# Performance work log

Hardware: AMD Instinct MI355X
Metric: run time of the kernel (lower is better)

Reference implementation:

```python
import jax, jax.numpy as jnp
import numpy as np

L, H, D, N, M, P, C, IMG, B = 12, 12, 768, 197, 3072, 16, 3, 224, 16
SKIP_AT = (3, 6, 9, 12)


def pos_emb(n, d):
    i = jnp.arange(n, dtype=jnp.float32)[:, None]
    j = jnp.arange(d)[None, :]
    je = (j // 2) * 2  # j for even, j-1 for odd
    ang = i / jnp.power(10000.0, je.astype(jnp.float32) / d)
    return jnp.where(j % 2 == 0, jnp.sin(ang), jnp.cos(ang))  # [n, d]


def layer_norm(x, g, b):
    mu = x.mean(-1, keepdims=True)
    var = x.var(-1, keepdims=True)
    return (x - mu) / jnp.sqrt(var + 1e-5) * g + b


def setup_inputs() -> dict:
    key = jax.random.key(0)
    ks = jax.random.split(key, 16)
    s = 0.02
    f32 = jnp.float32
    return {
        "images": jax.random.normal(ks[0], (B, C, IMG, IMG), f32),
        "class_token": jax.random.uniform(ks[1], (1, D), f32),
        "Wp": jax.random.normal(ks[2], (D, P * P * C), f32) * s,
        "bp": jnp.zeros((D,), f32),
        "Wq": jax.random.normal(ks[3], (L, H, D, D), f32) * s,
        "bq": jnp.zeros((L, H, D), f32),
        "Wk": jax.random.normal(ks[4], (L, H, D, D), f32) * s,
        "bk": jnp.zeros((L, H, D), f32),
        "Wv": jax.random.normal(ks[5], (L, H, D, D), f32) * s,
        "bv": jnp.zeros((L, H, D), f32),
        "Wm": jax.random.normal(ks[6], (L, N, H * N), f32) * s,
        "bm": jnp.zeros((L, N), f32),
        "g1": jnp.ones((L, D), f32),
        "be1": jnp.zeros((L, D), f32),
        "W1": jax.random.normal(ks[7], (L, M, D), f32) * s,
        "b1": jnp.zeros((L, M), f32),
        "W2": jax.random.normal(ks[8], (L, D, M), f32) * s,
        "b2": jnp.zeros((L, D), f32),
        "g2": jnp.ones((L, D), f32),
        "be2": jnp.zeros((L, D), f32),
    }


def reference(images, class_token, Wp, bp, Wq, bq, Wk, bk, Wv, bv, Wm, bm,
              g1, be1, W1, b1, W2, b2, g2, be2):
    b = images.shape[0]
    Hn, Wn = IMG // P, IMG // P
    # einops 'b c (patch_x h) (patch_y w) -> b (h w) (patch_x patch_y c)'
    x = images.reshape(b, C, P, Hn, P, Wn).transpose(0, 3, 5, 2, 4, 1)
    patches = x.reshape(b, Hn * Wn, P * P * C)
    tokens = patches @ Wp.T + bp  # [b, N-1, D]
    cls = jnp.broadcast_to(class_token[None], (b, 1, D))
    out = jnp.concatenate([cls, tokens], axis=1) + pos_emb(N, D)[None]
    scale = 1.0 / jnp.sqrt(jnp.float32(N - 1))
    skips = []
    for l in range(L):
        x0 = out
        q = jnp.einsum('bnd,hed->bhne', x0, Wq[l]) + bq[l][None, :, None, :]
        k = jnp.einsum('bnd,hed->bhne', x0, Wk[l]) + bk[l][None, :, None, :]
        v = jnp.einsum('bnd,hed->bhne', x0, Wv[l]) + bv[l][None, :, None, :]
        attn = jax.nn.softmax(jnp.einsum('bhne,bhme->bhnm', q, k) * scale, axis=-1)
        o = jnp.einsum('bhnm,bhme->bhne', attn, v).reshape(b, H * N, D)
        # transpose -> [b, D, H*N], Linear(H*N -> N), transpose back
        msa = jnp.einsum('bfd,nf->bnd', o, Wm[l]) + bm[l][None, :, None]
        x1 = layer_norm(x0 + msa, g1[l], be1[l])
        hdn = jax.nn.gelu(x1 @ W1[l].T + b1[l], approximate=False)
        out = layer_norm(x1 + (hdn @ W2[l].T + b2[l]), g2[l], be2[l])
        if l + 1 in SKIP_AT:
            skips.append(out[:, 1:, :])
    return (out[:, 1:, :], *skips)
```

## Files before the change

kernel.cpp:

```cpp
#include <hip/hip_runtime.h>
#include <cstdint>
#include <cstddef>

typedef __bf16 bf16;
typedef __bf16 bf16x8 __attribute__((ext_vector_type(8)));
typedef float f32x4 __attribute__((ext_vector_type(4)));

#define DEVINL __device__ __forceinline__

typedef const __attribute__((address_space(1))) void* as1cv;
typedef __attribute__((address_space(3))) void* as3v;

DEVINL void gload16(const bf16* g, bf16* l) {
    __builtin_amdgcn_global_load_lds((as1cv)g, (as3v)l, 16, 0, 0);
}

static constexpr int Lh = 12, Hh = 12, Dh = 768, Nh = 197, Mh = 3072, Bh = 16;
static constexpr int BN   = Bh * Nh;
static constexpr int NPAT = Bh * 196;
static constexpr int HD   = Hh * Dh;
static constexpr int QKN  = 2 * HD;
static constexpr int NP   = 256;
static constexpr int FHN  = Hh * Nh;
static constexpr int FP   = 2368;
static constexpr size_t SEC = (size_t)Bh * 196 * Dh;
static constexpr long LSqk = (long)QKN * Dh;
static constexpr long PART = (long)BN * Dh;

template<int AF32, int BF32, int OUTBF, int BIAS, int ACT, int ZFILL>
__global__ __launch_bounds__(256, 3) void gemm_bt(
    const void* __restrict__ Av, long sAy, long sAz, int lda,
    const void* __restrict__ Bv, long sBy, long sBz, int ldb,
    void* __restrict__ Cv, long sCy, long sCz, int ldc,
    const float* __restrict__ bias, long sBiasY,
    int Mv, int Nv, int K, int tilesN, int kChunk)
{
    __shared__ __align__(16) bf16 Asm[128 * 32];
    __shared__ __align__(16) bf16 Bsm[128 * 32];
    const int bx = blockIdx.x;
    const int tm = bx / tilesN, tn = bx % tilesN;
    const long aoff = (long)blockIdx.y * sAy + (long)blockIdx.z * sAz + (long)tm * 128 * lda;
    const long boff = (long)blockIdx.y * sBy + (long)blockIdx.z * sBz + (long)tn * 128 * ldb;
    const int tid = threadIdx.x;
    const int lane = tid & 63, wid = tid >> 6;
    const int ar = tid >> 2, ac = (tid & 3) << 3;
    const bf16* Ag = (const bf16*)Av + aoff + (long)ar * lda + ac;
    const bf16* Bg = (const bf16*)Bv + boff + (long)ar * ldb + ac;
    const float* Af = (const float*)Av + aoff + (long)ar * lda + ac;
    const float* Bf = (const float*)Bv + boff + (long)ar * ldb + ac;
    bf16* lA = Asm + wid * 512;
    bf16* lB = Bsm + wid * 512;
    const int mw = (wid >> 1) * 64, nw = (wid & 1) * 64;
    const int fr = lane & 15, fq = lane >> 4;
    const int kBeg = kChunk ? blockIdx.y * kChunk : 0;
    const int kEnd = kChunk ? min(K, kBeg + kChunk) : K;
    f32x4 acc[4][4] = {};
    for (int k0 = kBeg; k0 < kEnd; k0 += 32) {
        if (AF32) {
            const float* p0 = Af + k0;
            const float* p1 = p0 + (long)64 * lda;
            f32x4 a0 = *(const f32x4*)p0, a1 = *(const f32x4*)(p0 + 4);
            f32x4 a2 = *(const f32x4*)p1, a3 = *(const f32x4*)(p1 + 4);
            bf16x8 r0, r1;
#pragma unroll
            for (int i = 0; i < 4; i++) { r0[i] = (bf16)a0[i]; r0[i + 4] = (bf16)a1[i];
                                          r1[i] = (bf16)a2[i]; r1[i + 4] = (bf16)a3[i]; }
            *(bf16x8*)&Asm[ar * 32 + ac] = r0;
            *(bf16x8*)&Asm[(ar + 64) * 32 + ac] = r1;
        } else {
            gload16(Ag + k0, lA);
            gload16(Ag + (long)64 * lda + k0, lA + 2048);
        }
        if (BF32) {
            const float* p0 = Bf + k0;
            const float* p1 = p0 + (long)64 * ldb;
            f32x4 a0 = *(const f32x4*)p0, a1 = *(const f32x4*)(p0 + 4);
            f32x4 a2 = *(const f32x4*)p1, a3 = *(const f32x4*)(p1 + 4);
            bf16x8 r0, r1;
#pragma unroll
            for (int i = 0; i < 4; i++) { r0[i] = (bf16)a0[i]; r0[i + 4] = (bf16)a1[i];
                                          r1[i] = (bf16)a2[i]; r1[i + 4] = (bf16)a3[i]; }
            *(bf16x8*)&Bsm[ar * 32 + ac] = r0;
            *(bf16x8*)&Bsm[(ar + 64) * 32 + ac] = r1;
        } else {
            gload16(Bg + k0, lB);
            gload16(Bg + (long)64 * ldb + k0, lB + 2048);
        }
        __syncthreads();
        bf16x8 af[4], bv[4];
#pragma unroll
        for (int i = 0; i < 4; i++) af[i] = *(const bf16x8*)&Asm[(mw + i * 16 + fr) * 32 + (fq << 3)];
#pragma unroll
        for (int j = 0; j < 4; j++) bv[j] = *(const bf16x8*)&Bsm[(nw + j * 16 + fr) * 32 + (fq << 3)];
#pragma unroll
        for (int i = 0; i < 4; i++)
#pragma unroll
            for (int j = 0; j < 4; j++)
                acc[i][j] = __builtin_amdgcn_mfma_f32_16x16x32_bf16(af[i], bv[j], acc[i][j], 0, 0, 0);
        __syncthreads();
    }
    const long cb = (long)blockIdx.y * sCy + (long)blockIdx.z * sCz;
    const float* biasp = bias ? bias + (long)blockIdx.y * sBiasY : nullptr;
#pragma unroll
    for (int i = 0; i < 4; i++) {
        const int row0 = tm * 128 + mw + i * 16 + fq * 4;
#pragma unroll
        for (int j = 0; j < 4; j++) {
            const int col = tn * 128 + nw + j * 16 + fr;
            const bool cok = (col < Nv);
            if (!cok && !ZFILL) continue;
            float bc = (BIAS == 1 && cok) ? biasp[col] : 0.f;
#pragma unroll
            for (int r = 0; r < 4; r++) {
                const int rr = row0 + r;
                if (rr >= Mv) continue;
                float v;
                if (cok) {
                    v = acc[i][j][r];
                    if (BIAS == 1) v += bc;
                    if (BIAS == 2) v += biasp[rr];
                    if (ACT) v = 0.5f * v * (1.f + erff(v * 0.70710678118654752f));
                } else v = 0.f;
                const long ci = cb + (long)rr * ldc + col;
                if (OUTBF) ((bf16*)Cv)[ci] = (bf16)v;
                else       ((float*)Cv)[ci] = v;
            }
        }
    }
}

__global__ __launch_bounds__(256) void cvt_k(const float* __restrict__ in, bf16* __restrict__ out, long n) {
    const long i = ((long)blockIdx.x * 256 + threadIdx.x) * 8;
    if (i >= n) return;
    f32x4 a = *(const f32x4*)(in + i);
    f32x4 b = *(const f32x4*)(in + i + 4);
    bf16x8 r;
#pragma unroll
    for (int j = 0; j < 4; j++) { r[j] = (bf16)a[j]; r[j + 4] = (bf16)b[j]; }
    *(bf16x8*)(out + i) = r;
}

__global__ __launch_bounds__(256) void cvt_s_k(const float* __restrict__ in, bf16* __restrict__ out,
                                               long perLayer, long dstStride, long dstOff, long total) {
    const long i = ((long)blockIdx.x * 256 + threadIdx.x) * 8;
    if (i >= total) return;
    const long l = i / perLayer, r = i % perLayer;
    f32x4 a = *(const f32x4*)(in + i);
    f32x4 b = *(const f32x4*)(in + i + 4);
    bf16x8 v;
#pragma unroll
    for (int j = 0; j < 4; j++) { v[j] = (bf16)a[j]; v[j + 4] = (bf16)b[j]; }
    *(bf16x8*)(out + l * dstStride + dstOff + r) = v;
}

__global__ void qkbias_k(const float* __restrict__ bq, const float* __restrict__ bk, float* __restrict__ dst) {
    const int idx = blockIdx.x * 256 + threadIdx.x;
    if (idx >= Lh * QKN) return;
    const int l = idx / QKN, c = idx % QKN;
    dst[idx] = (c < HD) ? bq[l * HD + c] : bk[l * HD + c - HD];
}

__global__ void patch_k(const float* __restrict__ images, bf16* __restrict__ patches) {
    const long idx = (long)blockIdx.x * 256 + threadIdx.x;
    if (idx >= (long)NPAT * Dh) return;
    const int r = (int)(idx / Dh), f = (int)(idx % Dh);
    const int b = r / 196, pi = r % 196, h = pi / 14, w = pi % 14;
    const int px = f / 48, rem = f % 48, py = rem / 3, c = rem % 3;
    patches[idx] = (bf16)images[(((long)(b * 3 + c) * 224) + px * 14 + h) * 224 + py * 14 + w];
}

__global__ void assemble_k(const float* __restrict__ tokens, const float* __restrict__ cls,
                           float* __restrict__ x, bf16* __restrict__ xbf) {
    const long idx = (long)blockIdx.x * 256 + threadIdx.x;
    if (idx >= (long)BN * Dh) return;
    const int r = (int)(idx / Dh), d = (int)(idx % Dh);
    const int b = r / Nh, n = r % Nh;
    const int je = d & ~1;
    const float ang = (float)n / powf(10000.f, (float)je / 768.f);
    const float pe = (d & 1) ? cosf(ang) : sinf(ang);
    const float val = (n == 0) ? (cls[d] + pe)
                               : (tokens[((long)b * 196 + (n - 1)) * Dh + d] + pe);
    x[idx] = val;
    xbf[idx] = (bf16)val;
}

__global__ void wmpad_k(const float* __restrict__ Wm, bf16* __restrict__ WmP) {
    const long idx = (long)blockIdx.x * 256 + threadIdx.x;
    if (idx >= (long)Lh * 256 * FP) return;
    const int l = (int)(idx / (256 * FP));
    const int rem = (int)(idx % (256 * FP));
    const int n = rem / FP, f = rem % FP;
    bf16 v = (bf16)0.f;
    if (n < Nh && f < FHN) v = (bf16)Wm[((long)l * Nh + n) * FHN + f];
    WmP[idx] = v;
}

__global__ void otpad_k(bf16* __restrict__ oT, int cb) {
    const int idx = blockIdx.x * 256 + threadIdx.x;
    if (idx >= cb * Dh * 4) return;
    const int b = idx / (Dh * 4), rem = idx % (Dh * 4), e = rem / 4, f = rem % 4;
    oT[((long)b * Dh + e) * FP + FHN + f] = (bf16)0.f;
}

__global__ __launch_bounds__(256) void softmax_k(const float* __restrict__ S, bf16* __restrict__ P) {
    const int tid = threadIdx.x, lane = tid & 63, wv = tid >> 6;
    const long rr = (long)blockIdx.x * 4 + wv;
    const int bh = (int)(rr / Nh), n = (int)(rr % Nh);
    const float* s = S + ((long)bh * Nh + n) * NP;
    bf16* p = P + ((long)bh * NP + n) * NP;
    float v[4]; float mx = -1e30f;
#pragma unroll
    for (int i = 0; i < 4; i++) {
        const int c = lane + i * 64;
        const float t = (c < Nh) ? s[c] * (1.f / 14.f) : -1e30f;
        v[i] = t; mx = fmaxf(mx, t);
    }
    for (int o = 32; o; o >>= 1) mx = fmaxf(mx, __shfl_xor(mx, o));
    float sum = 0.f;
#pragma unroll
    for (int i = 0; i < 4; i++) {
        const int c = lane + i * 64;
        v[i] = (c < Nh) ? expf(v[i] - mx) : 0.f;
        sum += v[i];
    }
    for (int o = 32; o; o >>= 1) sum += __shfl_xor(sum, o);
    const float inv = 1.f / sum;
#pragma unroll
    for (int i = 0; i < 4; i++) p[lane + i * 64] = (bf16)(v[i] * inv);
}

template<int BIAS_ROW, int NPART>
__global__ __launch_bounds__(256) void add_ln_k(
    const float* __restrict__ in1, const float* __restrict__ in2, long pstride,
    const float* __restrict__ bias, const float* __restrict__ gamma, const float* __restrict__ beta,
    float* __restrict__ outF, bf16* __restrict__ outBF,
    float* __restrict__ dst0, float* __restrict__ dst1)
{
    const int r = blockIdx.x;
    const int b = r / Nh, n = r % Nh;
    const long base = (long)r * Dh;
    const int tid = threadIdx.x;
    const float rowb = BIAS_ROW ? bias[n] : 0.f;
    float v[3]; float s = 0.f, s2 = 0.f;
#pragma unroll
    for (int i = 0; i < 3; i++) {
        const int d = tid + 256 * i;
        float t = in1[base + d] + (BIAS_ROW ? rowb : bias[d]);
#pragma unroll
        for (int pp = 0; pp < NPART; pp++) t += in2[pp * pstride + base + d];
        v[i] = t; s += t; s2 += t * t;
    }
    for (int o = 32; o; o >>= 1) { s += __shfl_xor(s, o); s2 += __shfl_xor(s2, o); }
    __shared__ float red[8];
    const int lane = tid & 63, wv = tid >> 6;
    if (lane == 0) { red[wv] = s; red[4 + wv] = s2; }
    __syncthreads();
    s  = red[0] + red[1] + red[2] + red[3];
    s2 = red[4] + red[5] + red[6] + red[7];
    const float mu = s * (1.f / 768.f);
    const float var = s2 * (1.f / 768.f) - mu * mu;
    const float rs = rsqrtf(var + 1e-5f);
    const long ob = ((long)b * 196 + (n - 1)) * Dh;
#pragma unroll
    for (int i = 0; i < 3; i++) {
        const int d = tid + 256 * i;
        const float y = (v[i] - mu) * rs * gamma[d] + beta[d];
        outF[base + d] = y;
        outBF[base + d] = (bf16)y;
        if (n > 0) {
            if (dst0) dst0[ob + d] = y;
            if (dst1) dst1[ob + d] = y;
        }
    }
}

static inline size_t al256(size_t x) { return (x + 255) & ~(size_t)255; }

extern "C" void kernel_launch(void* const* d_in, const int* in_sizes, int n_in,
                              void* d_out, int out_size, void* d_ws, size_t ws_size,
                              hipStream_t stream) {
    (void)in_sizes; (void)n_in; (void)out_size;
    const float* images = (const float*)d_in[0];
    const float* cls    = (const float*)d_in[1];
    const float* Wp     = (const float*)d_in[2];
    const float* bp     = (const float*)d_in[3];
    const float* Wq     = (const float*)d_in[4];
    const float* bq     = (const float*)d_in[5];
    const float* Wk     = (const float*)d_in[6];
    const float* bk     = (const float*)d_in[7];
    const float* Wv     = (const float*)d_in[8];
    const float* bv     = (const float*)d_in[9];
    const float* Wm     = (const float*)d_in[10];
    const float* bm     = (const float*)d_in[11];
    const float* g1     = (const float*)d_in[12];
    const float* be1    = (const float*)d_in[13];
    const float* W1     = (const float*)d_in[14];
    const float* b1     = (const float*)d_in[15];
    const float* W2     = (const float*)d_in[16];
    const float* b2     = (const float*)d_in[17];
    const float* g2     = (const float*)d_in[18];
    const float* be2    = (const float*)d_in[19];
    float* out = (float*)d_out;

    const size_t xB    = al256(3152ull * 768 * 4);
    const size_t xbfB  = al256(3328ull * 768 * 2);
    const size_t x1B   = al256(3152ull * 768 * 4);
    const size_t x1bfB = al256(3200ull * 768 * 2);
    const size_t msaB  = al256(4ull * PART * 4);
    const size_t mlp2B = al256(4ull * PART * 4);
    const size_t wmpB  = al256(12ull * 256 * FP * 2);
    const size_t qkbB  = al256((size_t)Lh * QKN * 4);
    const size_t persistB = xB + xbfB + x1B + x1bfB + msaB + mlp2B + wmpB + qkbB;
    const size_t hdnB  = al256(3200ull * 3072 * 2);
    const size_t preB  = al256(3200ull * 768 * 2) + al256(3136ull * 768 * 4);
    const size_t wqkvB = al256((size_t)Lh * HD * Dh * 2);
    const size_t w12B  = al256((size_t)Lh * Mh * Dh * 2);
    const size_t wpB   = al256(768ull * 768 * 2);
    const size_t weightsB = 3 * wqkvB + 2 * w12B + wpB;

    auto chunk_bytes = [&](int cb, size_t& qbB_o, size_t& vtB_o, size_t& sB_o) -> size_t {
        const size_t qbRows = (size_t)((cb * 197 + 127) / 128 + 1) * 128;
        size_t qbB = al256(qbRows * HD * 2);
        size_t vtB = al256((size_t)cb * Hh * Dh * NP * 2);
        size_t sB  = al256((size_t)cb * Hh * Nh * NP * 4);
        size_t c = 2 * qbB + vtB + sB;
        if (c < hdnB) c = hdnB;
        if (c < preB) c = preB;
        qbB_o = qbB; vtB_o = vtB; sB_o = sB;
        return c;
    };
    const size_t margin = (size_t)(8u << 20);
    const size_t pBf  = al256((size_t)Bh * Hh * NP * NP * 2);
    const size_t otBf = al256((size_t)Bh * Dh * FP * 2);
    size_t qbBf, vtBf, sBf;
    size_t chunkF = chunk_bytes(16, qbBf, vtBf, sBf) + pBf + otBf;
    bool fused = (chunkF + persistB + weightsB + margin <= ws_size);

    int CB = 16; bool useCvt = true;
    size_t qbB, vtB, sB, chunkB;
    if (fused) {
        chunkB = chunkF; qbB = qbBf; vtB = vtBf; sB = sBf;
    } else {
        for (;;) {
            chunkB = chunk_bytes(CB, qbB, vtB, sB);
            if (chunkB + persistB + weightsB + margin <= ws_size) break;
            if (CB == 1) { useCvt = false; break; }
            CB >>= 1;
        }
        if (!useCvt) {
            CB = 16;
            for (;;) {
                chunkB = chunk_bytes(CB, qbB, vtB, sB);
                if (chunkB + persistB + margin <= ws_size || CB == 1) break;
                CB >>= 1;
            }
        }
    }

    char* wsb = (char*)d_ws;
    bf16*  qb  = (bf16*)wsb;
    bf16*  kb  = (bf16*)(wsb + qbB);
    bf16*  vT  = (bf16*)(wsb + 2 * qbB);
    float* S   = (float*)(wsb + 2 * qbB + vtB);
    bf16*  P2  = (bf16*)(wsb + 2 * qbB + vtB + sB);
    bf16*  oT2 = (bf16*)(wsb + 2 * qbB + vtB + sB + pBf);
    bf16*  oT  = fused ? oT2 : qb;
    bf16*  P   = fused ? P2  : kb;
    bf16*  hdn = (bf16*)wsb;
    bf16*  patches = (bf16*)wsb;
    float* tokens  = (float*)(wsb + al256(3200ull * 768 * 2));
    char* p = wsb + chunkB;
    float* x    = (float*)p; p += xB;
    bf16*  xbf  = (bf16*) p; p += xbfB;
    float* x1   = (float*)p; p += x1B;
    bf16*  x1bf = (bf16*) p; p += x1bfB;
    float* msaP = (float*)p; p += msaB;
    float* mlp2P= (float*)p; p += mlp2B;
    bf16*  WmP  = (bf16*) p; p += wmpB;
    float* qkbiasF = (float*)p; p += qkbB;
    bf16 *WqkB = nullptr, *WvB = nullptr, *W1B = nullptr, *W2B = nullptr, *WpB = nullptr;
    const bool cvt = fused || useCvt;
    if (cvt) {
        WqkB = (bf16*)p; p += 2 * wqkvB;
        WvB  = (bf16*)p; p += wqkvB;
        W1B  = (bf16*)p; p += w12B;
        W2B  = (bf16*)p; p += w12B;
        WpB  = (bf16*)p; p += wpB;
    }

    if (cvt) {
        const long nqkv = (long)Lh * HD * Dh;
        const long n12  = (long)Lh * Mh * Dh;
        const int gq = (int)((nqkv / 8 + 255) / 256);
        const int g12 = (int)((n12 / 8 + 255) / 256);
        cvt_s_k<<<gq, 256, 0, stream>>>(Wq, WqkB, (long)HD * Dh, LSqk, 0, nqkv);
        cvt_s_k<<<gq, 256, 0, stream>>>(Wk, WqkB, (long)HD * Dh, LSqk, (long)HD * Dh, nqkv);
        cvt_k<<<gq, 256, 0, stream>>>(Wv, WvB, nqkv);
        cvt_k<<<g12, 256, 0, stream>>>(W1, W1B, n12);
        cvt_k<<<g12, 256, 0, stream>>>(W2, W2B, n12);
        cvt_k<<<(768 * 768 / 8 + 255) / 256, 256, 0, stream>>>(Wp, WpB, 768 * 768);
        qkbias_k<<<(Lh * QKN + 255) / 256, 256, 0, stream>>>(bq, bk, qkbiasF);
    }

    patch_k<<<9408, 256, 0, stream>>>(images, patches);
    if (cvt)
        gemm_bt<0, 0, 0, 1, 0, 0><<<dim3(25 * 6), 256, 0, stream>>>(
            patches, 0, 0, 768, WpB, 0, 0, 768, tokens, 0, 0, 768, bp, 0, NPAT, 768, 768, 6, 0);
    else
        gemm_bt<0, 1, 0, 1, 0, 0><<<dim3(25 * 6), 256, 0, stream>>>(
            patches, 0, 0, 768, Wp, 0, 0, 768, tokens, 0, 0, 768, bp, 0, NPAT, 768, 768, 6, 0);
    assemble_k<<<9456, 256, 0, stream>>>(tokens, cls, x, xbf);
    wmpad_k<<<28416, 256, 0, stream>>>(Wm, WmP);
    if (fused) otpad_k<<<16 * 12, 256, 0, stream>>>(oT2, 16);

    const int NCH = 16 / CB;
    const int tilesQ = (CB * 197 + 127) / 128;

    for (int l = 0; l < 12; l++) {
        const float* Wq_l = Wq + (size_t)l * HD * Dh;
        const float* Wk_l = Wk + (size_t)l * HD * Dh;
        const float* Wv_l = Wv + (size_t)l * HD * Dh;
        const bf16* WqkB_l = cvt ? WqkB + (size_t)l * LSqk : nullptr;
        const bf16* WqB_l = WqkB_l;
        const bf16* WkB_l = cvt ? WqkB_l + (size_t)HD * Dh : nullptr;
        const bf16* WvB_l = cvt ? WvB + (size_t)l * HD * Dh : nullptr;
        const float* bq_l = bq + (size_t)l * HD;
        const float* bk_l = bk + (size_t)l * HD;
        const float* bv_l = bv + (size_t)l * HD;
        const bf16*  WmP_l = WmP + (size_t)l * 256 * FP;
        const float* bm_l = bm + (size_t)l * Nh;
        const float* g1_l = g1 + (size_t)l * Dh;  const float* be1_l = be1 + (size_t)l * Dh;
        const float* W1_l = W1 + (size_t)l * Mh * Dh; const float* b1_l = b1 + (size_t)l * Mh;
        const float* W2_l = W2 + (size_t)l * Dh * Mh; const float* b2_l = b2 + (size_t)l * Dh;
        const bf16* W1B_l = cvt ? W1B + (size_t)l * Mh * Dh : nullptr;
        const bf16* W2B_l = cvt ? W2B + (size_t)l * Mh * Dh : nullptr;
        const float* g2_l = g2 + (size_t)l * Dh;  const float* be2_l = be2 + (size_t)l * Dh;

        if (fused) {
            gemm_bt<0, 0, 1, 1, 0, 0><<<dim3(25 * 144), 256, 0, stream>>>(
                xbf, 0, 0, 768, WqkB_l, 0, 0, 768, qb, 0, 0, QKN,
                qkbiasF + (size_t)l * QKN, 0, BN, QKN, 768, 144, 0);
            gemm_bt<0, 0, 1, 2, 0, 1><<<dim3(12, 12, 16), 256, 0, stream>>>(
                WvB_l, (long)Dh * Dh, 0, 768,
                xbf, 0, (long)Nh * Dh, 768,
                vT, (long)Dh * NP, (long)Hh * Dh * NP, NP,
                bv_l, Dh, 768, Nh, 768, 2, 0);
            gemm_bt<0, 0, 0, 0, 0, 0><<<dim3(4, 12, 16), 256, 0, stream>>>(
                qb, 768, (long)Nh * QKN, QKN,
                qb + HD, 768, (long)Nh * QKN, QKN,
                S, (long)Nh * NP, (long)Hh * Nh * NP, NP,
                nullptr, 0, Nh, Nh, 768, 2, 0);
            softmax_k<<<16 * 591, 256, 0, stream>>>(S, P);
            gemm_bt<0, 0, 1, 0, 0, 0><<<dim3(12, 12, 16), 256, 0, stream>>>(
                vT, (long)Dh * NP, (long)Hh * Dh * NP, NP,
                P, (long)NP * NP, (long)Hh * NP * NP, NP,
                oT, (long)Nh, (long)Dh * FP, FP,
                nullptr, 0, Dh, Nh, NP, 2, 0);
            gemm_bt<0, 0, 0, 0, 0, 0><<<dim3(12, 4, 16), 256, 0, stream>>>(
                WmP_l, 0, 0, FP,
                oT, 0, (long)Dh * FP, FP,
                msaP, PART, (long)Nh * Dh, Dh,
                nullptr, 0, Nh, Dh, FP, 6, 608);
        } else {
            for (int c = 0; c < NCH; c++) {
                const size_t r0 = (size_t)c * CB * Nh;
                if (useCvt) {
                    gemm_bt<0, 0, 1, 1, 0, 0><<<dim3(tilesQ * 72), 256, 0, stream>>>(
                        xbf + r0 * Dh, 0, 0, 768, WqB_l, 0, 0, 768, qb, 0, 0, HD, bq_l, 0, CB * Nh, HD, 768, 72, 0);
                    gemm_bt<0, 0, 1, 1, 0, 0><<<dim3(tilesQ * 72), 256, 0, stream>>>(
                        xbf + r0 * Dh, 0, 0, 768, WkB_l, 0, 0, 768, kb, 0, 0, HD, bk_l, 0, CB * Nh, HD, 768, 72, 0);
                    gemm_bt<0, 0, 1, 2, 0, 1><<<dim3(12, 12, CB), 256, 0, stream>>>(
                        WvB_l, (long)Dh * Dh, 0, 768,
                        xbf + r0 * Dh, 0, (long)Nh * Dh, 768,
                        vT, (long)Dh * NP, (long)Hh * Dh * NP, NP,
                        bv_l, Dh, 768, Nh, 768, 2, 0);
                } else {
                    gemm_bt<0, 1, 1, 1, 0, 0><<<dim3(tilesQ * 72), 256, 0, stream>>>(
                        xbf + r0 * Dh, 0, 0, 768, Wq_l, 0, 0, 768, qb, 0, 0, HD, bq_l, 0, CB * Nh, HD, 768, 72, 0);
                    gemm_bt<0, 1, 1, 1, 0, 0><<<dim3(tilesQ * 72), 256, 0, stream>>>(
                        xbf + r0 * Dh, 0, 0, 768, Wk_l, 0, 0, 768, kb, 0, 0, HD, bk_l, 0, CB * Nh, HD, 768, 72, 0);
                    gemm_bt<1, 0, 1, 2, 0, 1><<<dim3(12, 12, CB), 256, 0, stream>>>(
                        Wv_l, (long)Dh * Dh, 0, 768,
                        xbf + r0 * Dh, 0, (long)Nh * Dh, 768,
                        vT, (long)Dh * NP, (long)Hh * Dh * NP, NP,
                        bv_l, Dh, 768, Nh, 768, 2, 0);
                }
                gemm_bt<0, 0, 0, 0, 0, 0><<<dim3(4, 12, CB), 256, 0, stream>>>(
                    qb, Dh, (long)Nh * HD, HD,
                    kb, Dh, (long)Nh * HD, HD,
                    S, (long)Nh * NP, (long)Hh * Nh * NP, NP,
                    nullptr, 0, Nh, Nh, 768, 2, 0);
                softmax_k<<<CB * 591, 256, 0, stream>>>(S, P);
                otpad_k<<<CB * 12, 256, 0, stream>>>(oT, CB);
                gemm_bt<0, 0, 1, 0, 0, 0><<<dim3(12, 12, CB), 256, 0, stream>>>(
                    vT, (long)Dh * NP, (long)Hh * Dh * NP, NP,
                    P, (long)NP * NP, (long)Hh * NP * NP, NP,
                    oT, (long)Nh, (long)Dh * FP, FP,
                    nullptr, 0, Dh, Nh, NP, 2, 0);
                gemm_bt<0, 0, 0, 0, 0, 0><<<dim3(12, 4, CB), 256, 0, stream>>>(
                    WmP_l, 0, 0, FP,
                    oT, 0, (long)Dh * FP, FP,
                    msaP + r0 * Dh, PART, (long)Nh * Dh, Dh,
                    nullptr, 0, Nh, Dh, FP, 6, 608);
            }
        }
        add_ln_k<1, 4><<<BN, 256, 0, stream>>>(x, msaP, PART, bm_l, g1_l, be1_l, x1, x1bf, nullptr, nullptr);
        if (cvt) {
            gemm_bt<0, 0, 1, 1, 1, 0><<<dim3(25 * 24), 256, 0, stream>>>(
                x1bf, 0, 0, 768, W1B_l, 0, 0, 768, hdn, 0, 0, Mh, b1_l, 0, BN, Mh, 768, 24, 0);
            gemm_bt<0, 0, 0, 0, 0, 0><<<dim3(25 * 6, 4, 1), 256, 0, stream>>>(
                hdn, 0, 0, Mh, W2B_l, 0, 0, Mh, mlp2P, PART, 0, Dh, nullptr, 0, BN, Dh, Mh, 6, 768);
        } else {
            gemm_bt<0, 1, 1, 1, 1, 0><<<dim3(25 * 24), 256, 0, stream>>>(
                x1bf, 0, 0, 768, W1_l, 0, 0, 768, hdn, 0, 0, Mh, b1_l, 0, BN, Mh, 768, 24, 0);
            gemm_bt<0, 1, 0, 0, 0, 0><<<dim3(25 * 6, 4, 1), 256, 0, stream>>>(
                hdn, 0, 0, Mh, W2_l, 0, 0, Mh, mlp2P, PART, 0, Dh, nullptr, 0, BN, Dh, Mh, 6, 768);
        }
        float* d0 = nullptr; float* d1 = nullptr;
        if (l == 2)  d0 = out + 1 * SEC;
        if (l == 5)  d0 = out + 2 * SEC;
        if (l == 8)  d0 = out + 3 * SEC;
        if (l == 11) { d0 = out; d1 = out + 4 * SEC; }
        add_ln_k<0, 4><<<BN, 256, 0, stream>>>(x1, mlp2P, PART, b2_l, g2_l, be2_l, x, xbf, d0, d1);
    }
}
```

Baseline: 6.470 ms.

## Fuse QK^T score GEMM with row softmax into one kernel

Replaces the separate QK^T GEMM, which wrote fp32 scores to a buffer, and the standalone softmax kernel with one kernel. The new kernel computes a 128x256 score tile per block using MFMA, does the row max and sum reductions across waves through shared memory, and writes normalized bf16 probabilities directly. This removes the round trip of the score matrix through global memory and one launch per layer. The risk is that each block reads rows beyond 197 (padding rows of the Q/K buffer), and occupancy may be lower with only 2x12x16 blocks of 512 threads.

```diff
diff --git a/kernel.cpp b/kernel.cpp
--- a/kernel.cpp
+++ b/kernel.cpp
@@ -129,6 +129,110 @@
     }
 }
 
+__global__ __launch_bounds__(512, 2) void qksoft_k(
+    const bf16* __restrict__ qkb, bf16* __restrict__ P)
+{
+    __shared__ __align__(16) bf16 Qs[128 * 32];
+    __shared__ __align__(16) bf16 Ks[256 * 32];
+    __shared__ float redM[2][64][4];
+    __shared__ float redS[2][64][4];
+    const int rt = blockIdx.x, h = blockIdx.y, b = blockIdx.z;
+    const int tid = threadIdx.x;
+    const int lane = tid & 63, wid = tid >> 6;
+    const int wr = wid >> 2, wc = wid & 3;
+    const int fr = lane & 15, fq = lane >> 4;
+    const int ar = tid >> 2, ac = (tid & 3) << 3;
+    const bf16* Qg = qkb + ((size_t)b * Nh + rt * 128 + ar) * QKN + h * Dh + ac;
+    const bf16* Kg = qkb + ((size_t)b * Nh + ar) * QKN + HD + h * Dh + ac;
+    bf16* lQ = Qs + wid * 512;
+    bf16* lK = Ks + wid * 512;
+    f32x4 acc[4][4] = {};
+    for (int k0 = 0; k0 < 768; k0 += 32) {
+        gload16(Qg + k0, lQ);
+        gload16(Kg + k0, lK);
+        gload16(Kg + (size_t)128 * QKN + k0, lK + 4096);
+        __syncthreads();
+        bf16x8 af[4], bv[4];
+#pragma unroll
+        for (int i = 0; i < 4; i++) af[i] = *(const bf16x8*)&Qs[(wr * 64 + i * 16 + fr) * 32 + (fq << 3)];
+#pragma unroll
+        for (int j = 0; j < 4; j++) bv[j] = *(const bf16x8*)&Ks[(wc * 64 + j * 16 + fr) * 32 + (fq << 3)];
+#pragma unroll
+        for (int i = 0; i < 4; i++)
+#pragma unroll
+            for (int j = 0; j < 4; j++)
+                acc[i][j] = __builtin_amdgcn_mfma_f32_16x16x32_bf16(af[i], bv[j], acc[i][j], 0, 0, 0);
+        __syncthreads();
+    }
+    const float scale = 1.f / 14.f;
+    float mx[4][4];
+#pragma unroll
+    for (int i = 0; i < 4; i++)
+#pragma unroll
+        for (int r = 0; r < 4; r++) {
+            float m0 = -3e30f;
+#pragma unroll
+            for (int j = 0; j < 4; j++) {
+                const int m = wc * 64 + j * 16 + fr;
+                float v = (m < Nh) ? acc[i][j][r] * scale : -3e30f;
+                acc[i][j][r] = v;
+                m0 = fmaxf(m0, v);
+            }
+            m0 = fmaxf(m0, __shfl_xor(m0, 1));
+            m0 = fmaxf(m0, __shfl_xor(m0, 2));
+            m0 = fmaxf(m0, __shfl_xor(m0, 4));
+            m0 = fmaxf(m0, __shfl_xor(m0, 8));
+            mx[i][r] = m0;
+        }
+    if (fr == 0) {
+#pragma unroll
+        for (int i = 0; i < 4; i++)
+#pragma unroll
+            for (int r = 0; r < 4; r++) redM[wr][i * 16 + fq * 4 + r][wc] = mx[i][r];
+    }
+    __syncthreads();
+    float sm[4][4];
+#pragma unroll
+    for (int i = 0; i < 4; i++)
+#pragma unroll
+        for (int r = 0; r < 4; r++) {
+            const int row = i * 16 + fq * 4 + r;
+            const float rm = fmaxf(fmaxf(redM[wr][row][0], redM[wr][row][1]),
+                                   fmaxf(redM[wr][row][2], redM[wr][row][3]));
+            float s0 = 0.f;
+#pragma unroll
+            for (int j = 0; j < 4; j++) {
+                const float e = expf(acc[i][j][r] - rm);
+                acc[i][j][r] = e;
+                s0 += e;
+            }
+            s0 += __shfl_xor(s0, 1);
+            s0 += __shfl_xor(s0, 2);
+            s0 += __shfl_xor(s0, 4);
+            s0 += __shfl_xor(s0, 8);
+            sm[i][r] = s0;
+        }
+    if (fr == 0) {
+#pragma unroll
+        for (int i = 0; i < 4; i++)
+#pragma unroll
+            for (int r = 0; r < 4; r++) redS[wr][i * 16 + fq * 4 + r][wc] = sm[i][r];
+    }
+    __syncthreads();
+    bf16* Pb = P + ((size_t)(b * Hh + h) * NP + rt * 128) * NP;
+#pragma unroll
+    for (int i = 0; i < 4; i++)
+#pragma unroll
+        for (int r = 0; r < 4; r++) {
+            const int row = i * 16 + fq * 4 + r;
+            const float s = redS[wr][row][0] + redS[wr][row][1] + redS[wr][row][2] + redS[wr][row][3];
+            const float inv = 1.f / s;
+#pragma unroll
+            for (int j = 0; j < 4; j++)
+                Pb[(size_t)(wr * 64 + row) * NP + wc * 64 + j * 16 + fr] = (bf16)(acc[i][j][r] * inv);
+        }
+}
+
 __global__ __launch_bounds__(256) void cvt_k(const float* __restrict__ in, bf16* __restrict__ out, long n) {
     const long i = ((long)blockIdx.x * 256 + threadIdx.x) * 8;
     if (i >= n) return;
@@ -445,12 +549,7 @@
                 xbf, 0, (long)Nh * Dh, 768,
                 vT, (long)Dh * NP, (long)Hh * Dh * NP, NP,
                 bv_l, Dh, 768, Nh, 768, 2, 0);
-            gemm_bt<0, 0, 0, 0, 0, 0><<<dim3(4, 12, 16), 256, 0, stream>>>(
-                qb, 768, (long)Nh * QKN, QKN,
-                qb + HD, 768, (long)Nh * QKN, QKN,
-                S, (long)Nh * NP, (long)Hh * Nh * NP, NP,
-                nullptr, 0, Nh, Nh, 768, 2, 0);
-            softmax_k<<<16 * 591, 256, 0, stream>>>(S, P);
+            qksoft_k<<<dim3(2, Hh, Bh), 512, 0, stream>>>(qb, P);
             gemm_bt<0, 0, 1, 0, 0, 0><<<dim3(12, 12, 16), 256, 0, stream>>>(
                 vT, (long)Dh * NP, (long)Hh * Dh * NP, NP,
                 P, (long)NP * NP, (long)Hh * NP * NP, NP,
```

Result: faster. 6.228 ms (-3.7%).
